# Kernel tuning notes

Hardware: AMD Instinct MI355X
Metric: run time of the kernel (lower is better)

## Reference

```python
import jax, jax.numpy as jnp
import numpy as np

N_NODES = 100000
N_EDGES = 1600000
IN_DIM = 256
OUT_DIM = 128
EPS = 1e-12  # torch F.normalize default eps


def setup_inputs() -> dict:
    key = jax.random.key(0)
    k1, k2, k3, k4, k5 = jax.random.split(key, 5)
    x = jax.random.normal(k1, (N_NODES, IN_DIM), dtype=jnp.float32)
    edge_index = jax.random.randint(k2, (2, N_EDGES), 0, N_NODES, dtype=jnp.int64)
    # projection (no bias): weight [out, in]
    Wp = jax.random.normal(k3, (OUT_DIM, IN_DIM), dtype=jnp.float32) * 0.05
    # GCNConv internal linear weight [out, out] and output bias [out]
    Wg = jax.random.normal(k4, (OUT_DIM, OUT_DIM), dtype=jnp.float32) * 0.05
    bg = jax.random.normal(k5, (OUT_DIM,), dtype=jnp.float32) * 0.01
    return {"x": x, "edge_index": edge_index, "Wp": Wp, "Wg": Wg, "bg": bg}


def reference(x, edge_index, Wp, Wg, bg):
    n = x.shape[0]
    # projection: x @ Wp^T
    h = x @ Wp.T                      # [N, OUT]
    # GCNConv: transform first, then propagate
    h = h @ Wg.T                      # [N, OUT]
    # add self-loops
    loops = jnp.arange(n, dtype=edge_index.dtype)
    row = jnp.concatenate([edge_index[0], loops])   # source
    col = jnp.concatenate([edge_index[1], loops])   # target
    # symmetric normalization: deg over target index (edge_weight = 1)
    deg = jax.ops.segment_sum(jnp.ones_like(col, dtype=h.dtype), col, num_segments=n)
    dinv = jnp.where(deg > 0, jax.lax.rsqrt(deg), 0.0)
    norm = dinv[row] * dinv[col]                     # [E+N]
    # gather messages from source, scale, scatter-add to target
    msg = h[row] * norm[:, None]                     # [E+N, OUT]
    out = jax.ops.segment_sum(msg, col, num_segments=n)  # [N, OUT]
    out = out + bg
    # F.normalize(dim=1): divide by L2 norm clamped at eps
    nrm = jnp.sqrt(jnp.sum(out * out, axis=1, keepdims=True))
    out = out / jnp.maximum(nrm, EPS)
    return out
```

## Files before the change

### kernel.cpp

```cpp
#include <hip/hip_runtime.h>
#include <hip/hip_fp16.h>

#define NDIM 128
#define KDIM 256
#define MT 5
#define AROW 264
#define CHUNK 6400
#define MAXBUCK 128

typedef _Float16 half8 __attribute__((ext_vector_type(8)));
typedef float float4v __attribute__((ext_vector_type(4)));

__global__ void k_combine_w(const float* __restrict__ Wp, const float* __restrict__ Wg,
                            _Float16* __restrict__ Bfrag) {
    int o = blockIdx.x;
    int i = threadIdx.x;
    float acc = 0.f;
#pragma unroll 4
    for (int k = 0; k < 128; ++k) acc = fmaf(Wg[o * 128 + k], Wp[k * 256 + i], acc);
    int kk = i >> 5, r = i & 31, quad = r >> 3, j = r & 7;
    int ntile = o >> 4, lanen = o & 15, lane = quad * 16 + lanen;
    Bfrag[(((ntile * 8 + kk) * 64) + lane) * 8 + j] = (_Float16)acc;
}

__global__ __launch_bounds__(256) void k_phase1(const int* __restrict__ col, int E,
                                                int* __restrict__ hist, int NBLK, int NBUCK) {
    __shared__ int h[MAXBUCK];
    int tid = threadIdx.x;
    if (tid < MAXBUCK) h[tid] = 0;
    __syncthreads();
    int e0 = blockIdx.x * CHUNK;
    int e1 = min(e0 + CHUNK, E);
    for (int e = e0 + tid; e < e1; e += 256) atomicAdd(&h[col[e] >> 10], 1);
    __syncthreads();
    if (tid < NBUCK) hist[tid * NBLK + blockIdx.x] = h[tid];
}

__global__ __launch_bounds__(1024) void k_scan2(int* __restrict__ hist, int NE) {
    __shared__ int s[1024];
    int t = threadIdx.x;
    int CH = (NE + 1023) >> 10;
    int off = t * CH;
    int sum = 0;
    for (int j = 0; j < CH; ++j) { int idx = off + j; if (idx < NE) sum += hist[idx]; }
    s[t] = sum;
    __syncthreads();
    for (int d = 1; d < 1024; d <<= 1) {
        int y = (t >= d) ? s[t - d] : 0;
        __syncthreads();
        s[t] += y;
        __syncthreads();
    }
    int run = s[t] - sum;
    for (int j = 0; j < CH; ++j) {
        int idx = off + j;
        if (idx < NE) { int v = hist[idx]; hist[idx] = run; run += v; }
    }
}

__global__ __launch_bounds__(256) void k_phase3(const int* __restrict__ ei, int E,
                                                const int* __restrict__ offs, int NBLK, int NBUCK,
                                                int2* __restrict__ tmp) {
    __shared__ int cur[MAXBUCK];
    int tid = threadIdx.x;
    if (tid < NBUCK) cur[tid] = offs[tid * NBLK + blockIdx.x];
    __syncthreads();
    int e0 = blockIdx.x * CHUNK;
    int e1 = min(e0 + CHUNK, E);
    for (int e = e0 + tid; e < e1; e += 256) {
        int r = ei[e];
        int c = ei[E + e];
        int p = atomicAdd(&cur[c >> 10], 1);
        tmp[p] = make_int2(r, c);
    }
}

__global__ __launch_bounds__(1024) void k_fine(const int2* __restrict__ tmp,
                                               const int* __restrict__ offs, int NBLK, int NBUCK,
                                               int N, int E,
                                               int* __restrict__ sortedRow,
                                               int* __restrict__ cnt,
                                               int* __restrict__ rowStart) {
    __shared__ int scnt[1024];
    __shared__ int cur[1024];
    int b = blockIdx.x;
    int t = threadIdx.x;
    int nodeBase = b << 10;
    int start = offs[b * NBLK];
    int end = (b + 1 < NBUCK) ? offs[(b + 1) * NBLK] : E;

    scnt[t] = 0;
    __syncthreads();
    for (int p = start + t; p < end; p += 1024) atomicAdd(&scnt[tmp[p].y - nodeBase], 1);
    __syncthreads();
    int v = scnt[t];
    for (int d = 1; d < 1024; d <<= 1) {
        int y = (t >= d) ? scnt[t - d] : 0;
        __syncthreads();
        scnt[t] += y;
        __syncthreads();
    }
    int excl = scnt[t] - v;
    int node = nodeBase + t;
    if (node < N) {
        cnt[node] = v;
        rowStart[node] = start + excl;
    }
    cur[t] = start + excl;
    __syncthreads();
    for (int p = start + t; p < end; p += 1024) {
        int2 pr = tmp[p];
        int slot = atomicAdd(&cur[pr.y - nodeBase], 1);
        sortedRow[slot] = pr.x;
    }
    if (b == NBUCK - 1 && t == 0) rowStart[N] = E;
}

__global__ __launch_bounds__(256) void k_gemm_mfma(const float* __restrict__ x,
                                                   const _Float16* __restrict__ Bfrag,
                                                   const int* __restrict__ cnt,
                                                   _Float16* __restrict__ g, int nrows) {
    __shared__ __align__(16) _Float16 xs[16 * AROW];
    int tid  = threadIdx.x;
    int lane = tid & 63;
    int w    = tid >> 6;
    int quad = lane >> 4;
    int lcol = lane & 15;

    const half8* Bv = (const half8*)Bfrag;
    half8 b0[8], b1[8];
#pragma unroll
    for (int kk = 0; kk < 8; ++kk) {
        b0[kk] = Bv[(w * 8 + kk) * 64 + lane];
        b1[kk] = Bv[((w + 4) * 8 + kk) * 64 + lane];
    }

    long base = (long)blockIdx.x * (16 * MT);
    for (int t = 0; t < MT; ++t) {
        long m0 = base + t * 16;
        __syncthreads();
        const float4* xv = (const float4*)(x + m0 * KDIM);
#pragma unroll
        for (int ii = 0; ii < 4; ++ii) {
            int idx = tid + ii * 256;
            int m = idx >> 6, k4 = idx & 63;
            float4 v = xv[idx];
            _Float16* d = &xs[m * AROW + k4 * 4];
            d[0] = (_Float16)v.x; d[1] = (_Float16)v.y;
            d[2] = (_Float16)v.z; d[3] = (_Float16)v.w;
        }
        __syncthreads();

        float4v acc0 = {0.f, 0.f, 0.f, 0.f}, acc1 = {0.f, 0.f, 0.f, 0.f};
#pragma unroll
        for (int kk = 0; kk < 8; ++kk) {
            half8 a = *(const half8*)(&xs[lcol * AROW + kk * 32 + quad * 8]);
            acc0 = __builtin_amdgcn_mfma_f32_16x16x32_f16(a, b0[kk], acc0, 0, 0, 0);
            acc1 = __builtin_amdgcn_mfma_f32_16x16x32_f16(a, b1[kk], acc1, 0, 0, 0);
        }

#pragma unroll
        for (int r = 0; r < 4; ++r) {
            long node = m0 + quad * 4 + r;
            float di = rsqrtf((float)(cnt[node] + 1));
            g[node * NDIM + w * 16 + lcol]        = (_Float16)(acc0[r] * di);
            g[node * NDIM + (w + 4) * 16 + lcol]  = (_Float16)(acc1[r] * di);
        }
    }
}

__global__ __launch_bounds__(256) void k_gather(const __half2* __restrict__ g,
                                                const int* __restrict__ rowStart,
                                                const int* __restrict__ sortedRow,
                                                const int* __restrict__ cnt,
                                                const float* __restrict__ bg,
                                                float* __restrict__ out) {
    int lane = threadIdx.x & 63;
    int i = blockIdx.x * 4 + (threadIdx.x >> 6);
    const int s = rowStart[i];
    const int e = rowStart[i + 1];
    const size_t stride = NDIM / 2;

    __half2 self = g[(size_t)i * stride + lane];
    float ax = __low2float(self), ay = __high2float(self);

    int p = s;
    for (; p + 4 <= e; p += 4) {
        int r0 = sortedRow[p + 0];
        int r1 = sortedRow[p + 1];
        int r2 = sortedRow[p + 2];
        int r3 = sortedRow[p + 3];
        __half2 m0 = g[(size_t)r0 * stride + lane];
        __half2 m1 = g[(size_t)r1 * stride + lane];
        __half2 m2 = g[(size_t)r2 * stride + lane];
        __half2 m3 = g[(size_t)r3 * stride + lane];
        ax += __low2float(m0) + __low2float(m1) + __low2float(m2) + __low2float(m3);
        ay += __high2float(m0) + __high2float(m1) + __high2float(m2) + __high2float(m3);
    }
    for (; p < e; ++p) {
        int r = sortedRow[p];
        __half2 m = g[(size_t)r * stride + lane];
        ax += __low2float(m);
        ay += __high2float(m);
    }

    float di = rsqrtf((float)(cnt[i] + 1));
    float2 b = ((const float2*)bg)[lane];
    float v0 = fmaf(di, ax, b.x);
    float v1 = fmaf(di, ay, b.y);

    float sq = v0 * v0 + v1 * v1;
#pragma unroll
    for (int d = 32; d > 0; d >>= 1) sq += __shfl_xor(sq, d);
    float scale = 1.0f / fmaxf(sqrtf(sq), 1e-12f);
    ((float2*)out)[(size_t)i * stride + lane] = make_float2(v0 * scale, v1 * scale);
}

extern "C" void kernel_launch(void* const* d_in, const int* in_sizes, int n_in,
                              void* d_out, int out_size, void* d_ws, size_t ws_size,
                              hipStream_t stream) {
    const float* x  = (const float*)d_in[0];
    const int*   ei = (const int*)  d_in[1];
    const float* Wp = (const float*)d_in[2];
    const float* Wg = (const float*)d_in[3];
    const float* bg = (const float*)d_in[4];
    float* out = (float*)d_out;

    const int N = in_sizes[0] / KDIM;
    const int E = in_sizes[1] / 2;

    const int NBLK  = (E + CHUNK - 1) / CHUNK;
    const int NBUCK = (N + 1023) >> 10;
    const int NE    = NBLK * NBUCK;

    char* p = (char*)d_ws;
    auto carve = [&](size_t bytes) { void* r = (void*)p; p += (bytes + 255) & ~(size_t)255; return r; };
    _Float16* g      = (_Float16*)carve((size_t)N * NDIM * 2);
    int*   sortedRow = (int*)  carve((size_t)E * 4);
    int2*  tmp       = (int2*) carve((size_t)E * 8);
    _Float16* Bfrag  = (_Float16*)carve((size_t)KDIM * NDIM * 2);
    int*   cnt       = (int*)  carve((size_t)N * 4);
    int*   rowStart  = (int*)  carve((size_t)(N + 1) * 4);
    int*   hist      = (int*)  carve((size_t)NE * 4);

    hipLaunchKernelGGL(k_combine_w, dim3(NDIM), dim3(KDIM), 0, stream, Wp, Wg, Bfrag);
    hipLaunchKernelGGL(k_phase1, dim3(NBLK), dim3(256), 0, stream, ei + E, E, hist, NBLK, NBUCK);
    hipLaunchKernelGGL(k_scan2, dim3(1), dim3(1024), 0, stream, hist, NE);
    hipLaunchKernelGGL(k_phase3, dim3(NBLK), dim3(256), 0, stream, ei, E, hist, NBLK, NBUCK, tmp);
    hipLaunchKernelGGL(k_fine, dim3(NBUCK), dim3(1024), 0, stream, tmp, hist, NBLK, NBUCK, N, E,
                       sortedRow, cnt, rowStart);
    hipLaunchKernelGGL(k_gemm_mfma, dim3(N / (16 * MT)), dim3(256), 0, stream, x, Bfrag, cnt, g, N);
    hipLaunchKernelGGL(k_gather, dim3(N / 4), dim3(256), 0, stream,
                       (const __half2*)g, rowStart, sortedRow, cnt, bg, out);
}
```

Before: 364.3 us.

## Double-buffer GEMM x tiles, split edge tmp arrays, stage targets in LDS, unroll gather

The GEMM kernel now double-buffers the LDS x tile, prefetching the next 16 rows into registers during the MFMAs, and doubles rows per block. The edge sort stores source and target in separate arrays, and the fine pass stages targets in shared memory so they are read from global memory only once. The gather loop unrolls to 8 neighbours to raise memory-level parallelism. The costs are extra LDS (about 96KB in k_fine, which lowers occupancy), more registers, and fewer GEMM blocks.

```diff
diff --git a/kernel.cpp b/kernel.cpp
--- a/kernel.cpp
+++ b/kernel.cpp
@@ -3,12 +3,14 @@
 
 #define NDIM 128
 #define KDIM 256
-#define MT 5
+#define MT 10
 #define AROW 264
 #define CHUNK 6400
 #define MAXBUCK 128
+#define SCAP 24576
 
 typedef _Float16 half8 __attribute__((ext_vector_type(8)));
+typedef _Float16 half4t __attribute__((ext_vector_type(4)));
 typedef float float4v __attribute__((ext_vector_type(4)));
 
 __global__ void k_combine_w(const float* __restrict__ Wp, const float* __restrict__ Wg,
@@ -60,7 +62,7 @@
 
 __global__ __launch_bounds__(256) void k_phase3(const int* __restrict__ ei, int E,
                                                 const int* __restrict__ offs, int NBLK, int NBUCK,
-                                                int2* __restrict__ tmp) {
+                                                int* __restrict__ tmpS, int* __restrict__ tmpT) {
     __shared__ int cur[MAXBUCK];
     int tid = threadIdx.x;
     if (tid < NBUCK) cur[tid] = offs[tid * NBLK + blockIdx.x];
@@ -71,11 +73,13 @@
         int r = ei[e];
         int c = ei[E + e];
         int p = atomicAdd(&cur[c >> 10], 1);
-        tmp[p] = make_int2(r, c);
-    }
-}
-
-__global__ __launch_bounds__(1024) void k_fine(const int2* __restrict__ tmp,
+        tmpS[p] = r;
+        tmpT[p] = c;
+    }
+}
+
+__global__ __launch_bounds__(1024) void k_fine(const int* __restrict__ tmpS,
+                                               const int* __restrict__ tmpT,
                                                const int* __restrict__ offs, int NBLK, int NBUCK,
                                                int N, int E,
                                                int* __restrict__ sortedRow,
@@ -83,15 +87,24 @@
                                                int* __restrict__ rowStart) {
     __shared__ int scnt[1024];
     __shared__ int cur[1024];
+    __shared__ int stg[SCAP];
     int b = blockIdx.x;
     int t = threadIdx.x;
     int nodeBase = b << 10;
     int start = offs[b * NBLK];
     int end = (b + 1 < NBUCK) ? offs[(b + 1) * NBLK] : E;
+    int len = end - start;
+    int nst = min(len, SCAP);
 
     scnt[t] = 0;
     __syncthreads();
-    for (int p = start + t; p < end; p += 1024) atomicAdd(&scnt[tmp[p].y - nodeBase], 1);
+    for (int j = t; j < nst; j += 1024) {
+        int tg = tmpT[start + j];
+        stg[j] = tg;
+        atomicAdd(&scnt[tg - nodeBase], 1);
+    }
+    for (int j = nst + t; j < len; j += 1024)
+        atomicAdd(&scnt[tmpT[start + j] - nodeBase], 1);
     __syncthreads();
     int v = scnt[t];
     for (int d = 1; d < 1024; d <<= 1) {
@@ -108,10 +121,17 @@
     }
     cur[t] = start + excl;
     __syncthreads();
-    for (int p = start + t; p < end; p += 1024) {
-        int2 pr = tmp[p];
-        int slot = atomicAdd(&cur[pr.y - nodeBase], 1);
-        sortedRow[slot] = pr.x;
+    for (int j = t; j < nst; j += 1024) {
+        int tg = stg[j];
+        int src = tmpS[start + j];
+        int slot = atomicAdd(&cur[tg - nodeBase], 1);
+        sortedRow[slot] = src;
+    }
+    for (int j = nst + t; j < len; j += 1024) {
+        int tg = tmpT[start + j];
+        int src = tmpS[start + j];
+        int slot = atomicAdd(&cur[tg - nodeBase], 1);
+        sortedRow[slot] = src;
     }
     if (b == NBUCK - 1 && t == 0) rowStart[N] = E;
 }
@@ -120,12 +140,14 @@
                                                    const _Float16* __restrict__ Bfrag,
                                                    const int* __restrict__ cnt,
                                                    _Float16* __restrict__ g, int nrows) {
-    __shared__ __align__(16) _Float16 xs[16 * AROW];
+    __shared__ __align__(16) _Float16 xs[2][16 * AROW];
     int tid  = threadIdx.x;
     int lane = tid & 63;
     int w    = tid >> 6;
     int quad = lane >> 4;
     int lcol = lane & 15;
+    int m_   = tid >> 6;
+    (void)m_;
 
     const half8* Bv = (const half8*)Bfrag;
     half8 b0[8], b1[8];
@@ -136,25 +158,38 @@
     }
 
     long base = (long)blockIdx.x * (16 * MT);
-    for (int t = 0; t < MT; ++t) {
-        long m0 = base + t * 16;
-        __syncthreads();
-        const float4* xv = (const float4*)(x + m0 * KDIM);
+    int sm = tid >> 6;
+    (void)sm;
+
+    float4 v[4];
+    {
+        const float4* xv = (const float4*)(x + base * KDIM);
+#pragma unroll
+        for (int ii = 0; ii < 4; ++ii) v[ii] = xv[tid + ii * 256];
 #pragma unroll
         for (int ii = 0; ii < 4; ++ii) {
             int idx = tid + ii * 256;
             int m = idx >> 6, k4 = idx & 63;
-            float4 v = xv[idx];
-            _Float16* d = &xs[m * AROW + k4 * 4];
-            d[0] = (_Float16)v.x; d[1] = (_Float16)v.y;
-            d[2] = (_Float16)v.z; d[3] = (_Float16)v.w;
-        }
-        __syncthreads();
+            half4t h; h[0] = (_Float16)v[ii].x; h[1] = (_Float16)v[ii].y;
+            h[2] = (_Float16)v[ii].z; h[3] = (_Float16)v[ii].w;
+            *(half4t*)&xs[0][m * AROW + k4 * 4] = h;
+        }
+    }
+    __syncthreads();
+
+    for (int t = 0; t < MT; ++t) {
+        int curb = t & 1, nxtb = curb ^ 1;
+        long m0 = base + t * 16;
+        if (t + 1 < MT) {
+            const float4* xn = (const float4*)(x + (m0 + 16) * KDIM);
+#pragma unroll
+            for (int ii = 0; ii < 4; ++ii) v[ii] = xn[tid + ii * 256];
+        }
 
         float4v acc0 = {0.f, 0.f, 0.f, 0.f}, acc1 = {0.f, 0.f, 0.f, 0.f};
 #pragma unroll
         for (int kk = 0; kk < 8; ++kk) {
-            half8 a = *(const half8*)(&xs[lcol * AROW + kk * 32 + quad * 8]);
+            half8 a = *(const half8*)(&xs[curb][lcol * AROW + kk * 32 + quad * 8]);
             acc0 = __builtin_amdgcn_mfma_f32_16x16x32_f16(a, b0[kk], acc0, 0, 0, 0);
             acc1 = __builtin_amdgcn_mfma_f32_16x16x32_f16(a, b1[kk], acc1, 0, 0, 0);
         }
@@ -166,6 +201,18 @@
             g[node * NDIM + w * 16 + lcol]        = (_Float16)(acc0[r] * di);
             g[node * NDIM + (w + 4) * 16 + lcol]  = (_Float16)(acc1[r] * di);
         }
+
+        if (t + 1 < MT) {
+#pragma unroll
+            for (int ii = 0; ii < 4; ++ii) {
+                int idx = tid + ii * 256;
+                int m = idx >> 6, k4 = idx & 63;
+                half4t h; h[0] = (_Float16)v[ii].x; h[1] = (_Float16)v[ii].y;
+                h[2] = (_Float16)v[ii].z; h[3] = (_Float16)v[ii].w;
+                *(half4t*)&xs[nxtb][m * AROW + k4 * 4] = h;
+            }
+        }
+        __syncthreads();
     }
 }
 
@@ -185,17 +232,27 @@
     float ax = __low2float(self), ay = __high2float(self);
 
     int p = s;
-    for (; p + 4 <= e; p += 4) {
+    for (; p + 8 <= e; p += 8) {
         int r0 = sortedRow[p + 0];
         int r1 = sortedRow[p + 1];
         int r2 = sortedRow[p + 2];
         int r3 = sortedRow[p + 3];
+        int r4 = sortedRow[p + 4];
+        int r5 = sortedRow[p + 5];
+        int r6 = sortedRow[p + 6];
+        int r7 = sortedRow[p + 7];
         __half2 m0 = g[(size_t)r0 * stride + lane];
         __half2 m1 = g[(size_t)r1 * stride + lane];
         __half2 m2 = g[(size_t)r2 * stride + lane];
         __half2 m3 = g[(size_t)r3 * stride + lane];
-        ax += __low2float(m0) + __low2float(m1) + __low2float(m2) + __low2float(m3);
-        ay += __high2float(m0) + __high2float(m1) + __high2float(m2) + __high2float(m3);
+        __half2 m4 = g[(size_t)r4 * stride + lane];
+        __half2 m5 = g[(size_t)r5 * stride + lane];
+        __half2 m6 = g[(size_t)r6 * stride + lane];
+        __half2 m7 = g[(size_t)r7 * stride + lane];
+        ax += __low2float(m0) + __low2float(m1) + __low2float(m2) + __low2float(m3)
+            + __low2float(m4) + __low2float(m5) + __low2float(m6) + __low2float(m7);
+        ay += __high2float(m0) + __high2float(m1) + __high2float(m2) + __high2float(m3)
+            + __high2float(m4) + __high2float(m5) + __high2float(m6) + __high2float(m7);
     }
     for (; p < e; ++p) {
         int r = sortedRow[p];
@@ -237,7 +294,8 @@
     auto carve = [&](size_t bytes) { void* r = (void*)p; p += (bytes + 255) & ~(size_t)255; return r; };
     _Float16* g      = (_Float16*)carve((size_t)N * NDIM * 2);
     int*   sortedRow = (int*)  carve((size_t)E * 4);
-    int2*  tmp       = (int2*) carve((size_t)E * 8);
+    int*   tmpS      = (int*)  carve((size_t)E * 4);
+    int*   tmpT      = (int*)  carve((size_t)E * 4);
     _Float16* Bfrag  = (_Float16*)carve((size_t)KDIM * NDIM * 2);
     int*   cnt       = (int*)  carve((size_t)N * 4);
     int*   rowStart  = (int*)  carve((size_t)(N + 1) * 4);
@@ -246,9 +304,9 @@
     hipLaunchKernelGGL(k_combine_w, dim3(NDIM), dim3(KDIM), 0, stream, Wp, Wg, Bfrag);
     hipLaunchKernelGGL(k_phase1, dim3(NBLK), dim3(256), 0, stream, ei + E, E, hist, NBLK, NBUCK);
     hipLaunchKernelGGL(k_scan2, dim3(1), dim3(1024), 0, stream, hist, NE);
-    hipLaunchKernelGGL(k_phase3, dim3(NBLK), dim3(256), 0, stream, ei, E, hist, NBLK, NBUCK, tmp);
-    hipLaunchKernelGGL(k_fine, dim3(NBUCK), dim3(1024), 0, stream, tmp, hist, NBLK, NBUCK, N, E,
-                       sortedRow, cnt, rowStart);
+    hipLaunchKernelGGL(k_phase3, dim3(NBLK), dim3(256), 0, stream, ei, E, hist, NBLK, NBUCK, tmpS, tmpT);
+    hipLaunchKernelGGL(k_fine, dim3(NBUCK), dim3(1024), 0, stream, tmpS, tmpT, hist, NBLK, NBUCK,
+                       N, E, sortedRow, cnt, rowStart);
     hipLaunchKernelGGL(k_gemm_mfma, dim3(N / (16 * MT)), dim3(256), 0, stream, x, Bfrag, cnt, g, N);
     hipLaunchKernelGGL(k_gather, dim3(N / 4), dim3(256), 0, stream,
                        (const __half2*)g, rowStart, sortedRow, cnt, bg, out);
```

Measured after the change: 368.8 us. Within noise of the previous version (+1.2%).
